# Kernel optimization log

Measured on AMD Instinct MI355X. Metric: run time of the kernel, lower is better.

The kernel has to match this reference:

```python
import jax, jax.numpy as jnp
import numpy as np

N = 100000   # nodes
IN = 128     # in_size
OUT = 64     # out_size (== out_size * layer_num_heads, heads=1)
P = 3        # meta-paths
E = 1600000  # edges per meta-path graph
HID = 32     # semantic attention hidden size


def setup_inputs() -> dict:
    key = jax.random.key(0)
    ks = jax.random.split(key, 8)
    h = jax.random.normal(ks[0], (N, IN), dtype=jnp.float32)
    edge_src = jax.random.randint(ks[1], (P, E), 0, N)
    edge_dst = jax.random.randint(ks[2], (P, E), 0, N)
    # xavier_uniform-style init for linear weights
    def xavier(k, shape):
        fan_in, fan_out = shape[0], shape[1]
        lim = np.sqrt(6.0 / (fan_in + fan_out)).astype(np.float32)
        return jax.random.uniform(k, shape, jnp.float32, -lim, lim)
    gc_w = xavier(ks[3], (IN, OUT))
    gc_b = jnp.zeros((OUT,), jnp.float32)
    sa_w1 = xavier(ks[4], (OUT, HID))
    sa_b1 = jnp.zeros((HID,), jnp.float32)
    sa_w2 = xavier(ks[5], (HID, 1))
    return {"h": h, "gc_w": gc_w, "gc_b": gc_b, "sa_w1": sa_w1,
            "sa_b1": sa_b1, "sa_w2": sa_w2,
            "edge_src": edge_src, "edge_dst": edge_dst}


def _graph_conv(h, gc_w, gc_b, src, dst):
    # DGL GraphConv, norm='both', activation=relu, allow_zero_in_degree.
    ones = jnp.ones(src.shape, h.dtype)
    out_deg = jax.ops.segment_sum(ones, src, num_segments=N)
    in_deg = jax.ops.segment_sum(ones, dst, num_segments=N)
    norm_src = jax.lax.rsqrt(jnp.maximum(out_deg, 1.0))  # [N]
    norm_dst = jax.lax.rsqrt(jnp.maximum(in_deg, 1.0))   # [N]
    # in_feats > out_feats: project first, then aggregate
    feat = (h * norm_src[:, None]) @ gc_w                # [N, OUT]
    agg = jax.ops.segment_sum(feat[src], dst, num_segments=N)  # [N, OUT]
    return jax.nn.relu(agg * norm_dst[:, None] + gc_b)


def reference(h, gc_w, gc_b, sa_w1, sa_b1, sa_w2, edge_src, edge_dst):
    # shared GraphConv applied to each meta-path graph (dropout p=0 -> identity)
    embs = [_graph_conv(h, gc_w, gc_b, edge_src[p], edge_dst[p]) for p in range(P)]
    z = jnp.stack(embs, axis=1)                          # [N, P, OUT]
    # semantic attention: small MLP -> mean over nodes -> softmax over meta-paths
    w = jnp.tanh(z @ sa_w1 + sa_b1) @ sa_w2              # [N, P, 1]
    beta = jax.nn.softmax(w.mean(axis=0), axis=0)        # [P, 1]
    out = (beta[None, :, :] * z).sum(axis=1)             # [N, OUT]
    return out, z
```

## Files before the change

kernel.cpp:

```cpp
#include <hip/hip_runtime.h>

#define NN 100000
#define IN_F 128
#define OUT_F 64
#define PP 3
#define EE 1600000
#define TOT (PP * EE)
#define HID 32
#define SEG_N (PP * NN)
#define NC1024 98
#define NCB (NC1024 * PP)
#define CAPC 17408
#define CHUNK 8192
#define NSX ((EE + CHUNK - 1) / CHUNK)
#define LCAP 64
#define NFB (NCB * 32)
#define WSLOTS 256

__device__ __forceinline__ unsigned short f2bf(float f) {
    unsigned u = __float_as_uint(f);
    u += 0x7FFFu + ((u >> 16) & 1u);
    return (unsigned short)(u >> 16);
}
__device__ __forceinline__ float bf2f(unsigned short b) {
    return __uint_as_float((unsigned)b << 16);
}
__device__ __forceinline__ float tanh_fast(float x) {
    float ax = fabsf(x);
    float e = __expf(-2.f * ax);
    float t = (1.f - e) / (1.f + e);
    return copysignf(t, x);
}

__global__ void __launch_bounds__(256) proj_kernel(const float* __restrict__ h,
                                                   const float* __restrict__ gc_w,
                                                   unsigned short* __restrict__ proj) {
    __shared__ float w_lds[IN_F * OUT_F];
    __shared__ float h_lds[32 * IN_F];
    int tid = threadIdx.x;
    for (int i = tid; i < IN_F * OUT_F / 4; i += 256)
        ((float4*)w_lds)[i] = ((const float4*)gc_w)[i];
    size_t r0 = (size_t)blockIdx.x * 32;
    for (int i = tid; i < 32 * IN_F / 4; i += 256)
        ((float4*)h_lds)[i] = ((const float4*)(h + r0 * IN_F))[i];
    __syncthreads();
    int wave = tid >> 6, lane = tid & 63;
    float acc[8] = {0.f, 0.f, 0.f, 0.f, 0.f, 0.f, 0.f, 0.f};
    for (int k = 0; k < IN_F; k += 4) {
        float w0 = w_lds[k * OUT_F + lane];
        float w1 = w_lds[(k + 1) * OUT_F + lane];
        float w2 = w_lds[(k + 2) * OUT_F + lane];
        float w3 = w_lds[(k + 3) * OUT_F + lane];
#pragma unroll
        for (int r = 0; r < 8; ++r) {
            float4 hv = *(const float4*)&h_lds[(wave * 8 + r) * IN_F + k];
            acc[r] = fmaf(hv.x, w0, fmaf(hv.y, w1, fmaf(hv.z, w2, fmaf(hv.w, w3, acc[r]))));
        }
    }
#pragma unroll
    for (int r = 0; r < 8; ++r)
        proj[(r0 + wave * 8 + r) * OUT_F + lane] = f2bf(acc[r]);
}

__global__ void scatter_coarse(const int* __restrict__ src, const int* __restrict__ dst,
                               unsigned* __restrict__ gcur_d, unsigned* __restrict__ gcur_s,
                               unsigned* __restrict__ gbuf_d, unsigned short* __restrict__ gbuf_s) {
    __shared__ unsigned cnt_d[4][NC1024], cnt_s[4][NC1024];
    int tid = threadIdx.x;
    int wv = tid >> 6;
    int p = blockIdx.y;
    for (int i = tid; i < 4 * NC1024; i += 256) { cnt_d[i / NC1024][i % NC1024] = 0u; cnt_s[i / NC1024][i % NC1024] = 0u; }
    __syncthreads();
    int e0 = blockIdx.x * CHUNK;
    const int* sp = src + (size_t)p * EE;
    const int* dp = dst + (size_t)p * EE;
    for (int i = 0; i < CHUNK / 256; ++i) {
        int e = e0 + i * 256 + tid;
        if (e < EE) {
            atomicAdd(&cnt_d[wv][dp[e] >> 10], 1u);
            atomicAdd(&cnt_s[wv][sp[e] >> 10], 1u);
        }
    }
    __syncthreads();
    for (int i = tid; i < NC1024; i += 256) {
        unsigned c0 = cnt_d[0][i], c1 = cnt_d[1][i], c2 = cnt_d[2][i], c3 = cnt_d[3][i];
        unsigned tt = c0 + c1 + c2 + c3;
        unsigned base = tt ? atomicAdd(&gcur_d[i * PP + p], tt) : 0u;
        cnt_d[0][i] = base; cnt_d[1][i] = base + c0;
        cnt_d[2][i] = base + c0 + c1; cnt_d[3][i] = base + c0 + c1 + c2;
        c0 = cnt_s[0][i]; c1 = cnt_s[1][i]; c2 = cnt_s[2][i]; c3 = cnt_s[3][i];
        tt = c0 + c1 + c2 + c3;
        base = tt ? atomicAdd(&gcur_s[i * PP + p], tt) : 0u;
        cnt_s[0][i] = base; cnt_s[1][i] = base + c0;
        cnt_s[2][i] = base + c0 + c1; cnt_s[3][i] = base + c0 + c1 + c2;
    }
    __syncthreads();
    for (int i = 0; i < CHUNK / 256; ++i) {
        int e = e0 + i * 256 + tid;
        if (e < EE) {
            int s = sp[e], d = dp[e];
            unsigned pd = atomicAdd(&cnt_d[wv][d >> 10], 1u);
            unsigned ps = atomicAdd(&cnt_s[wv][s >> 10], 1u);
            if (pd < CAPC) gbuf_d[(size_t)((d >> 10) * PP + p) * CAPC + pd] = (unsigned)s | ((unsigned)(d & 1023) << 17);
            if (ps < CAPC) gbuf_s[(size_t)((s >> 10) * PP + p) * CAPC + ps] = (unsigned short)(s & 1023);
        }
    }
}

__global__ void src_hist(const unsigned* __restrict__ gcur_s, const unsigned short* __restrict__ gbuf_s,
                         unsigned char* __restrict__ deg8) {
    __shared__ unsigned hist[4][1024];
    int tid = threadIdx.x;
    int wv = tid >> 6;
    for (int i = tid; i < 4 * 1024; i += 256) hist[i >> 10][i & 1023] = 0u;
    __syncthreads();
    int c = blockIdx.x;
    int blk = c / PP, p = c - blk * PP;
    unsigned cnt = gcur_s[c]; if (cnt > CAPC) cnt = CAPC;
    const unsigned short* gb = gbuf_s + (size_t)c * CAPC;
    for (unsigned j = tid; j < cnt; j += 256) atomicAdd(&hist[wv][gb[j]], 1u);
    __syncthreads();
    for (int i = tid; i < 1024; i += 256) {
        int n = blk * 1024 + i;
        unsigned hv = hist[0][i] + hist[1][i] + hist[2][i] + hist[3][i];
        if (n < NN) deg8[p * NN + n] = (unsigned char)(hv < 63u ? hv : 63u);
    }
}

__global__ void fine_split(const unsigned* __restrict__ gcur_d, const unsigned* __restrict__ gbuf_d,
                           const unsigned char* __restrict__ deg8, unsigned* __restrict__ gbuf_f,
                           unsigned* __restrict__ foff, unsigned* __restrict__ fcnt) {
    __shared__ unsigned hist[4][32], pre[32], cur[4][32];
    int c = blockIdx.x;
    int tid = threadIdx.x;
    int wv = tid >> 6;
    if (tid < 32) { hist[0][tid] = 0u; hist[1][tid] = 0u; hist[2][tid] = 0u; hist[3][tid] = 0u; }
    __syncthreads();
    int blk = c / PP, p = c - blk * PP;
    (void)blk;
    unsigned cnt = gcur_d[c]; if (cnt > CAPC) cnt = CAPC;
    const unsigned* gb = gbuf_d + (size_t)c * CAPC;
    for (unsigned j = tid; j < cnt; j += 256) atomicAdd(&hist[wv][gb[j] >> 22], 1u);
    __syncthreads();
    if (tid == 0) {
        unsigned a = 0;
        for (int i = 0; i < 32; ++i) {
            pre[i] = a;
            a += hist[0][i] + hist[1][i] + hist[2][i] + hist[3][i];
        }
    }
    __syncthreads();
    if (tid < 32) {
        unsigned a = pre[tid];
        cur[0][tid] = a; a += hist[0][tid];
        cur[1][tid] = a; a += hist[1][tid];
        cur[2][tid] = a; a += hist[2][tid];
        cur[3][tid] = a; a += hist[3][tid];
        foff[c * 32 + tid] = (unsigned)c * CAPC + pre[tid];
        fcnt[c * 32 + tid] = a - pre[tid];
    }
    __syncthreads();
    for (unsigned j = tid; j < cnt; j += 256) {
        unsigned v = gb[j];
        unsigned pos = atomicAdd(&cur[wv][v >> 22], 1u);
        unsigned s = v & 0x1FFFFu;
        unsigned node = (v >> 17) & 31u;
        unsigned dg = deg8[p * NN + s];
        gbuf_f[(size_t)c * CAPC + pos] = s | (node << 17) | (dg << 22);
    }
}

__global__ void __launch_bounds__(256, 8)
gather3c(const unsigned* __restrict__ foff, const unsigned* __restrict__ fcnt,
         const unsigned* __restrict__ gbuf_f, const unsigned short* __restrict__ proj,
         const float* __restrict__ gc_b, const float* __restrict__ sa_w1,
         const float* __restrict__ sa_b1, const float* __restrict__ sa_w2,
         float* __restrict__ zbuf, float* __restrict__ wsum) {
    __shared__ unsigned lists[32 * LCAP];
    __shared__ unsigned lcnt[32];
    __shared__ float zsh[4][OUT_F];
    int tid = threadIdx.x;
    int lane = tid & 63, wave = tid >> 6;
    int j = lane & 31, half = lane >> 5;
    unsigned w1p[16];
#pragma unroll
    for (int q = 0; q < 16; ++q) {
        float a = sa_w1[(half * 32 + 2 * q) * HID + j];
        float b = sa_w1[(half * 32 + 2 * q + 1) * HID + j];
        w1p[q] = (unsigned)f2bf(a) | ((unsigned)f2bf(b) << 16);
    }
    float b1r = sa_b1[j];
    float w2r = sa_w2[j];
    float bsr = gc_b[lane];
    if (tid < 32) lcnt[tid] = 0u;
    __syncthreads();

    int f = blockIdx.x;
    int c = f >> 5, sub = f & 31;
    int blk = c / PP, p = c - blk * PP;
    unsigned base = foff[f];
    unsigned cnt = fcnt[f];
    for (unsigned i = tid; i < cnt; i += 256) {
        unsigned v = gbuf_f[base + i];
        unsigned node = (v >> 17) & 31;
        unsigned sl = atomicAdd(&lcnt[node], 1u);
        if (sl < LCAP) lists[node * LCAP + sl] = v;
    }
    __syncthreads();

    int nbase = blk * 1024 + sub * 32;
    float logacc = 0.f;
    for (int k = 0; k < 8; ++k) {
        int node = wave * 8 + k;
        int n = nbase + node;
        if (n >= NN) continue;
        unsigned ind = lcnt[node];
        unsigned c2 = ind < LCAP ? ind : LCAP;
        unsigned pl = lists[node * LCAP + lane];
        float acc = 0.f;
        unsigned i = 0;
        for (; i + 4 <= c2; i += 4) {
            unsigned a0 = (unsigned)__builtin_amdgcn_readlane((int)pl, (int)i);
            unsigned a1 = (unsigned)__builtin_amdgcn_readlane((int)pl, (int)i + 1);
            unsigned a2 = (unsigned)__builtin_amdgcn_readlane((int)pl, (int)i + 2);
            unsigned a3 = (unsigned)__builtin_amdgcn_readlane((int)pl, (int)i + 3);
            float w0, w1w, w2w, w3w;
            float d0 = (float)((a0 >> 22) & 63u), d1 = (float)((a1 >> 22) & 63u);
            float d2 = (float)((a2 >> 22) & 63u), d3 = (float)((a3 >> 22) & 63u);
            asm("v_rsq_f32 %0, %1" : "=v"(w0) : "v"(d0));
            asm("v_rsq_f32 %0, %1" : "=v"(w1w) : "v"(d1));
            asm("v_rsq_f32 %0, %1" : "=v"(w2w) : "v"(d2));
            asm("v_rsq_f32 %0, %1" : "=v"(w3w) : "v"(d3));
            float p0 = bf2f(proj[(size_t)(a0 & 0x1FFFFu) * OUT_F + lane]);
            float p1 = bf2f(proj[(size_t)(a1 & 0x1FFFFu) * OUT_F + lane]);
            float p2 = bf2f(proj[(size_t)(a2 & 0x1FFFFu) * OUT_F + lane]);
            float p3 = bf2f(proj[(size_t)(a3 & 0x1FFFFu) * OUT_F + lane]);
            acc = fmaf(p0, w0, acc);
            acc = fmaf(p1, w1w, acc);
            acc = fmaf(p2, w2w, acc);
            acc = fmaf(p3, w3w, acc);
        }
        for (; i < c2; ++i) {
            unsigned a0 = (unsigned)__builtin_amdgcn_readlane((int)pl, (int)i);
            float d0 = (float)((a0 >> 22) & 63u);
            float w0; asm("v_rsq_f32 %0, %1" : "=v"(w0) : "v"(d0));
            acc = fmaf(bf2f(proj[(size_t)(a0 & 0x1FFFFu) * OUT_F + lane]), w0, acc);
        }
        float ndv = rsqrtf(fmaxf((float)ind, 1.f));
        float zv = fmaxf(fmaf(acc, ndv, bsr), 0.f);
        zbuf[((size_t)n * PP + p) * OUT_F + lane] = zv;
        zsh[wave][lane] = zv;
        float hp = 0.f;
        const float4* zrow = (const float4*)&zsh[wave][half * 32];
#pragma unroll
        for (int q = 0; q < 8; ++q) {
            float4 zq = zrow[q];
            unsigned u0 = w1p[2 * q], u1 = w1p[2 * q + 1];
            hp = fmaf(zq.x, __uint_as_float(u0 << 16), hp);
            hp = fmaf(zq.y, __uint_as_float(u0 & 0xFFFF0000u), hp);
            hp = fmaf(zq.z, __uint_as_float(u1 << 16), hp);
            hp = fmaf(zq.w, __uint_as_float(u1 & 0xFFFF0000u), hp);
        }
        hp += __shfl_xor(hp, 32);
        logacc += tanh_fast(hp + b1r) * w2r;
    }
#pragma unroll
    for (int off = 1; off < 64; off <<= 1) logacc += __shfl_xor(logacc, off);
    if (lane == 0) atomicAdd(&wsum[(blockIdx.x & (WSLOTS - 1)) * PP + p], logacc * 0.5f);
}

__global__ void beta_kernel(const float* __restrict__ wsum, float* __restrict__ beta) {
    if (threadIdx.x == 0) {
        float m[PP] = {0.f, 0.f, 0.f};
        for (int i = 0; i < WSLOTS; ++i)
            for (int p = 0; p < PP; ++p) m[p] += wsum[i * PP + p];
        float mx = -1e30f;
        for (int p = 0; p < PP; ++p) { m[p] *= (1.0f / NN); mx = fmaxf(mx, m[p]); }
        float e[PP], s = 0.f;
        for (int p = 0; p < PP; ++p) { e[p] = expf(m[p] - mx); s += e[p]; }
        for (int p = 0; p < PP; ++p) beta[p] = e[p] / s;
    }
}

__global__ void out_kernel(const float* __restrict__ zbuf, const float* __restrict__ beta,
                           float* __restrict__ out) {
    int t = blockIdx.x * 256 + threadIdx.x;
    if (t >= NN * (OUT_F / 4)) return;
    int n = t >> 4;
    int q = t & 15;
    float b0 = beta[0], b1 = beta[1], b2 = beta[2];
    const float4 v0 = ((const float4*)(zbuf + ((size_t)n * PP + 0) * OUT_F))[q];
    const float4 v1 = ((const float4*)(zbuf + ((size_t)n * PP + 1) * OUT_F))[q];
    const float4 v2 = ((const float4*)(zbuf + ((size_t)n * PP + 2) * OUT_F))[q];
    float4 r;
    r.x = b0 * v0.x + b1 * v1.x + b2 * v2.x;
    r.y = b0 * v0.y + b1 * v1.y + b2 * v2.y;
    r.z = b0 * v0.z + b1 * v1.z + b2 * v2.z;
    r.w = b0 * v0.w + b1 * v1.w + b2 * v2.w;
    ((float4*)out)[t] = r;
}

extern "C" void kernel_launch(void* const* d_in, const int* in_sizes, int n_in,
                              void* d_out, int out_size, void* d_ws, size_t ws_size,
                              hipStream_t stream) {
    const float* h     = (const float*)d_in[0];
    const float* gc_w  = (const float*)d_in[1];
    const float* gc_b  = (const float*)d_in[2];
    const float* sa_w1 = (const float*)d_in[3];
    const float* sa_b1 = (const float*)d_in[4];
    const float* sa_w2 = (const float*)d_in[5];
    const int* esrc    = (const int*)d_in[6];
    const int* edst    = (const int*)d_in[7];

    float* out  = (float*)d_out;
    unsigned short* proj = (unsigned short*)out;
    float* zbuf = out + (size_t)NN * OUT_F;

    char* ws = (char*)d_ws;
    const size_t OFF_GBD  = 0;
    const size_t OFF_GBS  = 20480000;
    const size_t OFF_GBF  = 20480000;
    const size_t OFF_DEG  = 41000000;
    const size_t OFF_FOFF = 41310000;
    const size_t OFF_FCNT = 41350000;
    const size_t OFF_GCD  = 41390000;
    const size_t OFF_GCS  = 41394096;
    const size_t OFF_WSUM = 41400000;
    const size_t OFF_BETA = 41410000;

    unsigned* gbuf_d       = (unsigned*)(ws + OFF_GBD);
    unsigned short* gbuf_s = (unsigned short*)(ws + OFF_GBS);
    unsigned* gbuf_f       = (unsigned*)(ws + OFF_GBF);
    unsigned char* deg8    = (unsigned char*)(ws + OFF_DEG);
    unsigned* foff         = (unsigned*)(ws + OFF_FOFF);
    unsigned* fcnt         = (unsigned*)(ws + OFF_FCNT);
    unsigned* gcur_d       = (unsigned*)(ws + OFF_GCD);
    unsigned* gcur_s       = (unsigned*)(ws + OFF_GCS);
    float* wsum            = (float*)(ws + OFF_WSUM);
    float* beta            = (float*)(ws + OFF_BETA);

    hipMemsetAsync(gcur_d, 0, NCB * sizeof(unsigned), stream);
    hipMemsetAsync(gcur_s, 0, NCB * sizeof(unsigned), stream);
    hipMemsetAsync(wsum, 0, WSLOTS * PP * sizeof(float), stream);

    proj_kernel<<<(NN + 31) / 32, 256, 0, stream>>>(h, gc_w, proj);
    scatter_coarse<<<dim3(NSX, PP), 256, 0, stream>>>(esrc, edst, gcur_d, gcur_s, gbuf_d, gbuf_s);
    src_hist<<<NCB, 256, 0, stream>>>(gcur_s, gbuf_s, deg8);
    fine_split<<<NCB, 256, 0, stream>>>(gcur_d, gbuf_d, deg8, gbuf_f, foff, fcnt);
    gather3c<<<NFB, 256, 0, stream>>>(foff, fcnt, gbuf_f, proj,
                                      gc_b, sa_w1, sa_b1, sa_w2, zbuf, wsum);
    beta_kernel<<<1, 64, 0, stream>>>(wsum, beta);
    out_kernel<<<(NN * (OUT_F / 4) + 255) / 256, 256, 0, stream>>>(zbuf, beta, out);
}
```

Before: 427.7 us.

## Fold source-degree normalization into per-metapath projection tables; drop per-edge rsqrt

The projection kernel now runs after the source-degree histogram and writes three bf16 tables, each pre-scaled by that meta-path's rsqrt(out-degree). The gather loop can then do plain adds with no per-edge degree decode or rsqrt. Degrees are also no longer clamped to 63 in a packed field. fine_split stages the bucket in LDS and sorts it back into the same buffer, removing the degree lookup and the separate output buffer. The cost is writing three projection tables instead of one, about three times the projection store traffic, and gathers now hit three separate tables.

```diff
diff --git a/kernel.cpp b/kernel.cpp
--- a/kernel.cpp
+++ b/kernel.cpp
@@ -32,36 +32,6 @@
     return copysignf(t, x);
 }
 
-__global__ void __launch_bounds__(256) proj_kernel(const float* __restrict__ h,
-                                                   const float* __restrict__ gc_w,
-                                                   unsigned short* __restrict__ proj) {
-    __shared__ float w_lds[IN_F * OUT_F];
-    __shared__ float h_lds[32 * IN_F];
-    int tid = threadIdx.x;
-    for (int i = tid; i < IN_F * OUT_F / 4; i += 256)
-        ((float4*)w_lds)[i] = ((const float4*)gc_w)[i];
-    size_t r0 = (size_t)blockIdx.x * 32;
-    for (int i = tid; i < 32 * IN_F / 4; i += 256)
-        ((float4*)h_lds)[i] = ((const float4*)(h + r0 * IN_F))[i];
-    __syncthreads();
-    int wave = tid >> 6, lane = tid & 63;
-    float acc[8] = {0.f, 0.f, 0.f, 0.f, 0.f, 0.f, 0.f, 0.f};
-    for (int k = 0; k < IN_F; k += 4) {
-        float w0 = w_lds[k * OUT_F + lane];
-        float w1 = w_lds[(k + 1) * OUT_F + lane];
-        float w2 = w_lds[(k + 2) * OUT_F + lane];
-        float w3 = w_lds[(k + 3) * OUT_F + lane];
-#pragma unroll
-        for (int r = 0; r < 8; ++r) {
-            float4 hv = *(const float4*)&h_lds[(wave * 8 + r) * IN_F + k];
-            acc[r] = fmaf(hv.x, w0, fmaf(hv.y, w1, fmaf(hv.z, w2, fmaf(hv.w, w3, acc[r]))));
-        }
-    }
-#pragma unroll
-    for (int r = 0; r < 8; ++r)
-        proj[(r0 + wave * 8 + r) * OUT_F + lane] = f2bf(acc[r]);
-}
-
 __global__ void scatter_coarse(const int* __restrict__ src, const int* __restrict__ dst,
                                unsigned* __restrict__ gcur_d, unsigned* __restrict__ gcur_s,
                                unsigned* __restrict__ gbuf_d, unsigned short* __restrict__ gbuf_s) {
@@ -108,7 +78,7 @@
 }
 
 __global__ void src_hist(const unsigned* __restrict__ gcur_s, const unsigned short* __restrict__ gbuf_s,
-                         unsigned char* __restrict__ deg8) {
+                         float* __restrict__ nsrc) {
     __shared__ unsigned hist[4][1024];
     int tid = threadIdx.x;
     int wv = tid >> 6;
@@ -123,24 +93,64 @@
     for (int i = tid; i < 1024; i += 256) {
         int n = blk * 1024 + i;
         unsigned hv = hist[0][i] + hist[1][i] + hist[2][i] + hist[3][i];
-        if (n < NN) deg8[p * NN + n] = (unsigned char)(hv < 63u ? hv : 63u);
-    }
-}
-
-__global__ void fine_split(const unsigned* __restrict__ gcur_d, const unsigned* __restrict__ gbuf_d,
-                           const unsigned char* __restrict__ deg8, unsigned* __restrict__ gbuf_f,
+        if (n < NN) nsrc[p * NN + n] = rsqrtf(fmaxf((float)hv, 1.f));
+    }
+}
+
+__global__ void __launch_bounds__(256) proj_fused(const float* __restrict__ h,
+                                                  const float* __restrict__ gc_w,
+                                                  const float* __restrict__ nsrc,
+                                                  unsigned short* __restrict__ t0,
+                                                  unsigned short* __restrict__ t1,
+                                                  unsigned short* __restrict__ t2) {
+    __shared__ float w_lds[IN_F * OUT_F];
+    __shared__ float h_lds[32 * IN_F];
+    int tid = threadIdx.x;
+    for (int i = tid; i < IN_F * OUT_F / 4; i += 256)
+        ((float4*)w_lds)[i] = ((const float4*)gc_w)[i];
+    size_t r0 = (size_t)blockIdx.x * 32;
+    for (int i = tid; i < 32 * IN_F / 4; i += 256)
+        ((float4*)h_lds)[i] = ((const float4*)(h + r0 * IN_F))[i];
+    __syncthreads();
+    int wave = tid >> 6, lane = tid & 63;
+    float acc[8] = {0.f, 0.f, 0.f, 0.f, 0.f, 0.f, 0.f, 0.f};
+    for (int k = 0; k < IN_F; k += 4) {
+        float w0 = w_lds[k * OUT_F + lane];
+        float w1 = w_lds[(k + 1) * OUT_F + lane];
+        float w2 = w_lds[(k + 2) * OUT_F + lane];
+        float w3 = w_lds[(k + 3) * OUT_F + lane];
+#pragma unroll
+        for (int r = 0; r < 8; ++r) {
+            float4 hv = *(const float4*)&h_lds[(wave * 8 + r) * IN_F + k];
+            acc[r] = fmaf(hv.x, w0, fmaf(hv.y, w1, fmaf(hv.z, w2, fmaf(hv.w, w3, acc[r]))));
+        }
+    }
+#pragma unroll
+    for (int r = 0; r < 8; ++r) {
+        size_t n = r0 + wave * 8 + r;
+        float a = acc[r];
+        t0[n * OUT_F + lane] = f2bf(a * nsrc[n]);
+        t1[n * OUT_F + lane] = f2bf(a * nsrc[NN + n]);
+        t2[n * OUT_F + lane] = f2bf(a * nsrc[2 * NN + n]);
+    }
+}
+
+__global__ void fine_split(const unsigned* __restrict__ gcur_d, unsigned* __restrict__ gbuf_d,
                            unsigned* __restrict__ foff, unsigned* __restrict__ fcnt) {
+    __shared__ unsigned stage[CAPC];
     __shared__ unsigned hist[4][32], pre[32], cur[4][32];
     int c = blockIdx.x;
     int tid = threadIdx.x;
     int wv = tid >> 6;
     if (tid < 32) { hist[0][tid] = 0u; hist[1][tid] = 0u; hist[2][tid] = 0u; hist[3][tid] = 0u; }
     __syncthreads();
-    int blk = c / PP, p = c - blk * PP;
-    (void)blk;
     unsigned cnt = gcur_d[c]; if (cnt > CAPC) cnt = CAPC;
-    const unsigned* gb = gbuf_d + (size_t)c * CAPC;
-    for (unsigned j = tid; j < cnt; j += 256) atomicAdd(&hist[wv][gb[j] >> 22], 1u);
+    unsigned* gb = gbuf_d + (size_t)c * CAPC;
+    for (unsigned j = tid; j < cnt; j += 256) {
+        unsigned v = gb[j];
+        stage[j] = v;
+        atomicAdd(&hist[wv][v >> 22], 1u);
+    }
     __syncthreads();
     if (tid == 0) {
         unsigned a = 0;
@@ -161,18 +171,17 @@
     }
     __syncthreads();
     for (unsigned j = tid; j < cnt; j += 256) {
-        unsigned v = gb[j];
+        unsigned v = stage[j];
         unsigned pos = atomicAdd(&cur[wv][v >> 22], 1u);
-        unsigned s = v & 0x1FFFFu;
-        unsigned node = (v >> 17) & 31u;
-        unsigned dg = deg8[p * NN + s];
-        gbuf_f[(size_t)c * CAPC + pos] = s | (node << 17) | (dg << 22);
+        gb[pos] = v & 0x3FFFFFu;
     }
 }
 
 __global__ void __launch_bounds__(256, 8)
-gather3c(const unsigned* __restrict__ foff, const unsigned* __restrict__ fcnt,
-         const unsigned* __restrict__ gbuf_f, const unsigned short* __restrict__ proj,
+gather3d(const unsigned* __restrict__ foff, const unsigned* __restrict__ fcnt,
+         const unsigned* __restrict__ gbuf_f,
+         const unsigned short* __restrict__ t0, const unsigned short* __restrict__ t1,
+         const unsigned short* __restrict__ t2,
          const float* __restrict__ gc_b, const float* __restrict__ sa_w1,
          const float* __restrict__ sa_b1, const float* __restrict__ sa_w2,
          float* __restrict__ zbuf, float* __restrict__ wsum) {
@@ -198,6 +207,7 @@
     int f = blockIdx.x;
     int c = f >> 5, sub = f & 31;
     int blk = c / PP, p = c - blk * PP;
+    const unsigned short* tp = (p == 0) ? t0 : (p == 1) ? t1 : t2;
     unsigned base = foff[f];
     unsigned cnt = fcnt[f];
     for (unsigned i = tid; i < cnt; i += 256) {
@@ -224,27 +234,15 @@
             unsigned a1 = (unsigned)__builtin_amdgcn_readlane((int)pl, (int)i + 1);
             unsigned a2 = (unsigned)__builtin_amdgcn_readlane((int)pl, (int)i + 2);
             unsigned a3 = (unsigned)__builtin_amdgcn_readlane((int)pl, (int)i + 3);
-            float w0, w1w, w2w, w3w;
-            float d0 = (float)((a0 >> 22) & 63u), d1 = (float)((a1 >> 22) & 63u);
-            float d2 = (float)((a2 >> 22) & 63u), d3 = (float)((a3 >> 22) & 63u);
-            asm("v_rsq_f32 %0, %1" : "=v"(w0) : "v"(d0));
-            asm("v_rsq_f32 %0, %1" : "=v"(w1w) : "v"(d1));
-            asm("v_rsq_f32 %0, %1" : "=v"(w2w) : "v"(d2));
-            asm("v_rsq_f32 %0, %1" : "=v"(w3w) : "v"(d3));
-            float p0 = bf2f(proj[(size_t)(a0 & 0x1FFFFu) * OUT_F + lane]);
-            float p1 = bf2f(proj[(size_t)(a1 & 0x1FFFFu) * OUT_F + lane]);
-            float p2 = bf2f(proj[(size_t)(a2 & 0x1FFFFu) * OUT_F + lane]);
-            float p3 = bf2f(proj[(size_t)(a3 & 0x1FFFFu) * OUT_F + lane]);
-            acc = fmaf(p0, w0, acc);
-            acc = fmaf(p1, w1w, acc);
-            acc = fmaf(p2, w2w, acc);
-            acc = fmaf(p3, w3w, acc);
+            float p0 = bf2f(tp[(size_t)(a0 & 0x1FFFFu) * OUT_F + lane]);
+            float p1 = bf2f(tp[(size_t)(a1 & 0x1FFFFu) * OUT_F + lane]);
+            float p2 = bf2f(tp[(size_t)(a2 & 0x1FFFFu) * OUT_F + lane]);
+            float p3 = bf2f(tp[(size_t)(a3 & 0x1FFFFu) * OUT_F + lane]);
+            acc += (p0 + p1) + (p2 + p3);
         }
         for (; i < c2; ++i) {
             unsigned a0 = (unsigned)__builtin_amdgcn_readlane((int)pl, (int)i);
-            float d0 = (float)((a0 >> 22) & 63u);
-            float w0; asm("v_rsq_f32 %0, %1" : "=v"(w0) : "v"(d0));
-            acc = fmaf(bf2f(proj[(size_t)(a0 & 0x1FFFFu) * OUT_F + lane]), w0, acc);
+            acc += bf2f(tp[(size_t)(a0 & 0x1FFFFu) * OUT_F + lane]);
         }
         float ndv = rsqrtf(fmaxf((float)ind, 1.f));
         float zv = fmaxf(fmaf(acc, ndv, bsr), 0.f);
@@ -313,25 +311,26 @@
     const int* edst    = (const int*)d_in[7];
 
     float* out  = (float*)d_out;
-    unsigned short* proj = (unsigned short*)out;
     float* zbuf = out + (size_t)NN * OUT_F;
+    unsigned short* t0 = (unsigned short*)out;
+    unsigned short* t1 = t0 + (size_t)NN * OUT_F;
 
     char* ws = (char*)d_ws;
     const size_t OFF_GBD  = 0;
     const size_t OFF_GBS  = 20480000;
-    const size_t OFF_GBF  = 20480000;
-    const size_t OFF_DEG  = 41000000;
-    const size_t OFF_FOFF = 41310000;
-    const size_t OFF_FCNT = 41350000;
-    const size_t OFF_GCD  = 41390000;
-    const size_t OFF_GCS  = 41394096;
-    const size_t OFF_WSUM = 41400000;
-    const size_t OFF_BETA = 41410000;
+    const size_t OFF_T2   = 20480000;
+    const size_t OFF_NSRC = 33300000;
+    const size_t OFF_FOFF = 34600000;
+    const size_t OFF_FCNT = 34650000;
+    const size_t OFF_GCD  = 34700000;
+    const size_t OFF_GCS  = 34710000;
+    const size_t OFF_WSUM = 34720000;
+    const size_t OFF_BETA = 34730000;
 
     unsigned* gbuf_d       = (unsigned*)(ws + OFF_GBD);
     unsigned short* gbuf_s = (unsigned short*)(ws + OFF_GBS);
-    unsigned* gbuf_f       = (unsigned*)(ws + OFF_GBF);
-    unsigned char* deg8    = (unsigned char*)(ws + OFF_DEG);
+    unsigned short* t2     = (unsigned short*)(ws + OFF_T2);
+    float* nsrc            = (float*)(ws + OFF_NSRC);
     unsigned* foff         = (unsigned*)(ws + OFF_FOFF);
     unsigned* fcnt         = (unsigned*)(ws + OFF_FCNT);
     unsigned* gcur_d       = (unsigned*)(ws + OFF_GCD);
@@ -343,11 +342,11 @@
     hipMemsetAsync(gcur_s, 0, NCB * sizeof(unsigned), stream);
     hipMemsetAsync(wsum, 0, WSLOTS * PP * sizeof(float), stream);
 
-    proj_kernel<<<(NN + 31) / 32, 256, 0, stream>>>(h, gc_w, proj);
     scatter_coarse<<<dim3(NSX, PP), 256, 0, stream>>>(esrc, edst, gcur_d, gcur_s, gbuf_d, gbuf_s);
-    src_hist<<<NCB, 256, 0, stream>>>(gcur_s, gbuf_s, deg8);
-    fine_split<<<NCB, 256, 0, stream>>>(gcur_d, gbuf_d, deg8, gbuf_f, foff, fcnt);
-    gather3c<<<NFB, 256, 0, stream>>>(foff, fcnt, gbuf_f, proj,
+    src_hist<<<NCB, 256, 0, stream>>>(gcur_s, gbuf_s, nsrc);
+    proj_fused<<<NN / 32, 256, 0, stream>>>(h, gc_w, nsrc, t0, t1, t2);
+    fine_split<<<NCB, 256, 0, stream>>>(gcur_d, gbuf_d, foff, fcnt);
+    gather3d<<<NFB, 256, 0, stream>>>(foff, fcnt, gbuf_d, t0, t1, t2,
                                       gc_b, sa_w1, sa_b1, sa_w2, zbuf, wsum);
     beta_kernel<<<1, 64, 0, stream>>>(wsum, beta);
     out_kernel<<<(NN * (OUT_F / 4) + 255) / 256, 256, 0, stream>>>(zbuf, beta, out);
```

Measured after the change: 391.3 us. 1.09x faster.
